# Optimization experiments

Hardware: AMD Instinct MI355X
Metric: run time of the kernel (lower is better)

## Reference

```python
import jax, jax.numpy as jnp
import numpy as np

K, N, MEM_D = 512, 4096, 64


def setup_inputs() -> dict:
    key = jax.random.key(0)
    k1, k2, k3, k4 = jax.random.split(key, 4)
    # event counts per location/time (torch code uses raw observations; rand in [0,1) keeps log-lik finite)
    obs = jax.random.uniform(k1, (K, N), jnp.float32)
    extobs = jax.random.normal(k2, (K, N), jnp.float32)
    beta = jnp.asarray(2.0, jnp.float32)  # torch.Tensor([2]) scalar rate parameter
    alpha = jax.random.uniform(k3, (K, K), jnp.float32, 0.0, 0.01)
    gamma = jax.random.uniform(k4, (K, MEM_D), jnp.float32, 0.0, 0.01)
    return {"obs": obs, "extobs": extobs, "beta": beta, "alpha": alpha, "gamma": gamma}


def reference(obs, extobs, beta, alpha, gamma):
    Kk, Nn = obs.shape
    d = gamma.shape[1]
    # mu is derived from obs exactly as in __init__ (not a trainable parameter)
    mu = obs.mean(axis=1) / 10.0 + 0.01  # [K]

    t = jnp.arange(Nn)
    diff = t[:, None] - t[None, :]  # [N, N], diff[t, j] = t - j
    # strict lower-triangular exponential decay kernel: D[t, j] = beta * exp(-(t-j)*beta) for j < t
    # clamp diff before exp so masked entries never produce inf (keeps vjp NaN-free)
    safe = jnp.maximum(diff, 1).astype(jnp.float32)
    Dmat = jnp.where(diff > 0, beta * jnp.exp(-safe * beta), 0.0)  # [N, N]

    # lam1[k, t] = sum_{k'} alpha[k, k'] * sum_{j < t} obs[k', j] * beta * exp(-(t-j)*beta)
    lam1 = alpha @ (obs @ Dmat.T)  # [K, N]

    # lam2[k, t] = sum_i extobs[k, t-d+i] * gamma[k, i]  (only when t >= d, else 0)
    # depthwise 1D cross-correlation with left zero-padding of d, then mask t < d
    x = extobs[None]            # [1, K, N]
    w = gamma[:, None, :]       # [K, 1, d]
    lam2 = jax.lax.conv_general_dilated(
        x, w, window_strides=(1,), padding=[(d, 0)],
        dimension_numbers=("NCH", "OIH", "NCH"), feature_group_count=Kk,
    )[0, :, :Nn]                # [K, N]
    lam2 = jnp.where(t[None, :] >= d, lam2, 0.0)

    lams = jax.nn.softplus(mu[:, None] + lam1 + lam2)  # [K, N]
    loglik = (obs * jnp.log(lams) - lams).sum()
    return (loglik, lams)
```

## Files before the change

kernel.cpp:

```cpp
#include <hip/hip_runtime.h>
#include <math.h>

#define KDIM 512
#define NDIM 4096
#define MEMD 64
#define WTAPS 16
#define SEG 1024
#define NSEG (NDIM / SEG)
#define NPART (KDIM * NSEG)

#define GBM 64
#define GBN 64
#define GBK 64

typedef short bf16x8 __attribute__((ext_vector_type(8)));
typedef float f32x4 __attribute__((ext_vector_type(4)));

#define GLOAD_LDS16(g, l) __builtin_amdgcn_global_load_lds( \
    (const __attribute__((address_space(1))) unsigned int*)(g), \
    (__attribute__((address_space(3))) unsigned int*)(l), 16, 0, 0)

__device__ __forceinline__ void bsplit(float a, ushort& hi, ushort& lo) {
    uint u = __float_as_uint(a);
    uint h = (u + 0x7FFFu + ((u >> 16) & 1u)) >> 16;
    hi = (ushort)h;
    float hf = __uint_as_float(h << 16);
    float r = a - hf;
    uint u2 = __float_as_uint(r);
    lo = (ushort)((u2 + 0x7FFFu + ((u2 >> 16) & 1u)) >> 16);
}

__device__ __forceinline__ float block_reduce_256(float v, float* sbuf) {
    #pragma unroll
    for (int off = 32; off > 0; off >>= 1) v += __shfl_down(v, off, 64);
    int lane = threadIdx.x & 63, wid = threadIdx.x >> 6;
    if (lane == 0) sbuf[wid] = v;
    __syncthreads();
    float tot = sbuf[0] + sbuf[1] + sbuf[2] + sbuf[3];
    __syncthreads();
    return tot;
}

__device__ __forceinline__ double block_reduce_256d(double v, double* dbuf) {
    #pragma unroll
    for (int off = 32; off > 0; off >>= 1) v += __shfl_down(v, off, 64);
    int lane = threadIdx.x & 63, wid = threadIdx.x >> 6;
    if (lane == 0) dbuf[wid] = v;
    __syncthreads();
    double tot = dbuf[0] + dbuf[1] + dbuf[2] + dbuf[3];
    __syncthreads();
    return tot;
}

__global__ __launch_bounds__(256) void conv_kernel(
    const float* __restrict__ B, const float* __restrict__ A,
    ushort* __restrict__ Bthi, ushort* __restrict__ Btlo,
    ushort* __restrict__ Ahi, ushort* __restrict__ Alo,
    float* __restrict__ mu) {
    __shared__ float s[64][65];
    int b = blockIdx.x, tid = threadIdx.x;
    if (b < 512) {
        int n0 = (b & 63) * 64, k0 = (b >> 6) * 64;
        #pragma unroll
        for (int i = 0; i < 4; ++i) {
            int idx = i * 256 + tid;
            int row = idx >> 4, c4 = idx & 15;
            float4 v = *(const float4*)&B[(size_t)(k0 + row) * NDIM + n0 + c4 * 4];
            s[row][c4 * 4 + 0] = v.x; s[row][c4 * 4 + 1] = v.y;
            s[row][c4 * 4 + 2] = v.z; s[row][c4 * 4 + 3] = v.w;
        }
        __syncthreads();
        #pragma unroll
        for (int i = 0; i < 2; ++i) {
            int idx = i * 256 + tid;
            int n = idx >> 3, k8 = idx & 7;
            ushort hs[8], ls[8];
            #pragma unroll
            for (int j = 0; j < 8; ++j) bsplit(s[k8 * 8 + j][n], hs[j], ls[j]);
            size_t o = (size_t)(n0 + n) * KDIM + k0 + k8 * 8;
            *(uint4*)&Bthi[o] = *(const uint4*)hs;
            *(uint4*)&Btlo[o] = *(const uint4*)ls;
        }
    } else if (b < 640) {
        int ab = b - 512;
        int g = ab * 256 + tid;
        const float4* src = (const float4*)A;
        #pragma unroll
        for (int i = 0; i < 2; ++i) {
            float4 v = src[g * 2 + i];
            ushort4 h, l;
            bsplit(v.x, h.x, l.x); bsplit(v.y, h.y, l.y);
            bsplit(v.z, h.z, l.z); bsplit(v.w, h.w, l.w);
            *(ushort4*)&Ahi[(size_t)g * 8 + i * 4] = h;
            *(ushort4*)&Alo[(size_t)g * 8 + i * 4] = l;
        }
    } else {
        int k = b - 640;
        const float* row = B + (size_t)k * NDIM;
        float ss = 0.f;
        for (int j = tid; j < NDIM; j += 256) ss += row[j];
        float tot = block_reduce_256(ss, &s[0][0]);
        if (tid == 0) mu[k] = tot / (float)NDIM / 10.0f + 0.01f;
    }
}

__global__ __launch_bounds__(256) void mfma_gemm(
    const ushort* __restrict__ Ahi, const ushort* __restrict__ Alo,
    const ushort* __restrict__ Bthi, const ushort* __restrict__ Btlo,
    float* __restrict__ C) {
    __shared__ __align__(16) ushort Asm[2][2][GBM * GBK];
    __shared__ __align__(16) ushort Bsm[2][2][GBN * GBK];
    int tid = threadIdx.x;
    int m0 = blockIdx.y * GBM, n0 = blockIdx.x * GBN;
    int l = tid & 63, w = tid >> 6;
    int wm = w >> 1, wn = w & 1;
    int lr = l & 15, lk = l >> 4;

    f32x4 acc[2][2];
    #pragma unroll
    for (int i = 0; i < 2; ++i)
        #pragma unroll
        for (int j = 0; j < 2; ++j) acc[i][j] = (f32x4){0.f, 0.f, 0.f, 0.f};

#define STAGE(bb, c0)                                                              \
    _Pragma("unroll")                                                              \
    for (int i_ = 0; i_ < 4; ++i_) {                                               \
        int c_ = tid + i_ * 256;                                                   \
        int plane_ = c_ >> 9, q_ = c_ & 511;                                       \
        int row_ = q_ >> 3, kc_ = (q_ & 7) ^ (row_ & 7);                           \
        const ushort* sa_ = (plane_ ? Alo : Ahi) + (size_t)(m0 + row_) * KDIM + (c0) + kc_ * 8; \
        GLOAD_LDS16(sa_, (char*)&Asm[bb][0][0] + c_ * 16);                         \
        const ushort* sb_ = (plane_ ? Btlo : Bthi) + (size_t)(n0 + row_) * KDIM + (c0) + kc_ * 8; \
        GLOAD_LDS16(sb_, (char*)&Bsm[bb][0][0] + c_ * 16);                         \
    }

    STAGE(0, 0);
    __syncthreads();

    for (int t = 0; t < 8; ++t) {
        int cur = t & 1;
        if (t < 7) { STAGE(cur ^ 1, (t + 1) * GBK); }

        bf16x8 ah[2][2], al[2][2], bh[2][2], bl[2][2];
        #pragma unroll
        for (int mf = 0; mf < 2; ++mf)
            #pragma unroll
            for (int s = 0; s < 2; ++s) {
                int ra = wm * 32 + mf * 16 + lr;
                int offa = ra * 128 + (((s * 64) + lk * 16) ^ ((ra & 7) << 4));
                ah[mf][s] = *(const bf16x8*)((const char*)&Asm[cur][0][0] + offa);
                al[mf][s] = *(const bf16x8*)((const char*)&Asm[cur][1][0] + offa);
                int rb = wn * 32 + mf * 16 + lr;
                int offb = rb * 128 + (((s * 64) + lk * 16) ^ ((rb & 7) << 4));
                bh[mf][s] = *(const bf16x8*)((const char*)&Bsm[cur][0][0] + offb);
                bl[mf][s] = *(const bf16x8*)((const char*)&Bsm[cur][1][0] + offb);
            }
        #pragma unroll
        for (int s = 0; s < 2; ++s)
            #pragma unroll
            for (int mf = 0; mf < 2; ++mf)
                #pragma unroll
                for (int nf = 0; nf < 2; ++nf) {
                    acc[mf][nf] = __builtin_amdgcn_mfma_f32_16x16x32_bf16(ah[mf][s], bh[nf][s], acc[mf][nf], 0, 0, 0);
                    acc[mf][nf] = __builtin_amdgcn_mfma_f32_16x16x32_bf16(ah[mf][s], bl[nf][s], acc[mf][nf], 0, 0, 0);
                    acc[mf][nf] = __builtin_amdgcn_mfma_f32_16x16x32_bf16(al[mf][s], bh[nf][s], acc[mf][nf], 0, 0, 0);
                }
        __syncthreads();
    }
#undef STAGE

    #pragma unroll
    for (int mf = 0; mf < 2; ++mf)
        #pragma unroll
        for (int nf = 0; nf < 2; ++nf)
            #pragma unroll
            for (int j = 0; j < 4; ++j) {
                int rm = m0 + wm * 32 + mf * 16 + lk * 4 + j;
                int cn = n0 + wn * 32 + nf * 16 + lr;
                C[(size_t)rm * NDIM + cn] = acc[mf][nf][j];
            }
}

__global__ __launch_bounds__(256) void final_kernel(
    const float* __restrict__ T, const float* __restrict__ obs,
    const float* __restrict__ extobs, const float* __restrict__ gamma,
    const float* __restrict__ beta_p, const float* __restrict__ mu,
    float* __restrict__ lams_out, double* __restrict__ partials) {
    __shared__ float Ts[SEG + 16];
    __shared__ float Es[SEG + 64];
    __shared__ float Os[SEG];
    __shared__ float Gs[MEMD];
    __shared__ float Wt[WTAPS];
    __shared__ double dbuf[4];

    int b = blockIdx.x, tid = threadIdx.x;
    int k = b >> 2, s = b & 3;
    float beta = *beta_p;
    float muk = mu[k];

    const float4* gT = (const float4*)(T + (size_t)k * NDIM);
    const float4* gE = (const float4*)(extobs + (size_t)k * NDIM);
    const float4* gO = (const float4*)(obs + (size_t)k * NDIM);
    float4 z = make_float4(0.f, 0.f, 0.f, 0.f);

    {
        for (int i = tid; i < 260; i += 256) {
            int gi = s * 256 - 4 + i;
            ((float4*)Ts)[i] = (gi >= 0) ? gT[gi] : z;
        }
        for (int i = tid; i < 272; i += 256) {
            int gi = s * 256 - 16 + i;
            ((float4*)Es)[i] = (gi >= 0) ? gE[gi] : z;
        }
        ((float4*)Os)[tid] = gO[s * 256 + tid];
        if (tid < MEMD) Gs[tid] = gamma[(size_t)k * MEMD + tid];
        if (tid >= 64 && tid < 64 + WTAPS) {
            int m = tid - 63;
            Wt[m - 1] = beta * expf(-beta * (float)m);
        }
    }
    __syncthreads();

    int t_loc = tid * 4;
    int t = s * SEG + t_loc;
    float win[20];
    float l1[4] = {0.f, 0.f, 0.f, 0.f};
    float l2[4] = {0.f, 0.f, 0.f, 0.f};

    #pragma unroll
    for (int c = 0; c < 5; ++c) *(float4*)&win[c * 4] = *(const float4*)&Ts[t_loc + c * 4];
    #pragma unroll
    for (int m = 1; m <= WTAPS; ++m) {
        float wm = Wt[m - 1];
        #pragma unroll
        for (int j = 0; j < 4; ++j) l1[j] = fmaf(wm, win[16 + j - m], l1[j]);
    }

    #pragma unroll
    for (int c4 = 0; c4 < 4; ++c4) {
        #pragma unroll
        for (int c = 0; c < 5; ++c)
            *(float4*)&win[c * 4] = *(const float4*)&Es[t_loc + c4 * 16 + c * 4];
        #pragma unroll
        for (int i = 0; i < 16; ++i) {
            float g = Gs[c4 * 16 + i];
            #pragma unroll
            for (int j = 0; j < 4; ++j) l2[j] = fmaf(g, win[i + j], l2[j]);
        }
    }
    if (t < MEMD) { l2[0] = 0.f; l2[1] = 0.f; l2[2] = 0.f; l2[3] = 0.f; }

    float4 o = ((const float4*)Os)[tid];
    float oo[4] = {o.x, o.y, o.z, o.w};
    double part = 0.0;
    f32x4 sv;
    #pragma unroll
    for (int j = 0; j < 4; ++j) {
        float x = muk + l1[j] + l2[j];
        float sp = fmaxf(x, 0.f) + log1pf(expf(-fabsf(x)));
        sv[j] = sp;
        part += (double)(oo[j] * logf(sp) - sp);
    }
    *(f32x4*)&lams_out[(size_t)k * NDIM + t] = sv;

    double dtot = block_reduce_256d(part, dbuf);
    if (tid == 0) partials[b] = dtot;
}

__global__ __launch_bounds__(256) void reduce_kernel(const double* __restrict__ partials,
                                                     float* __restrict__ out) {
    __shared__ double dbuf[4];
    double v = 0.0;
    for (int j = threadIdx.x; j < NPART; j += 256) v += partials[j];
    double tot = block_reduce_256d(v, dbuf);
    if (threadIdx.x == 0) out[0] = (float)tot;
}

extern "C" void kernel_launch(void* const* d_in, const int* in_sizes, int n_in,
                              void* d_out, int out_size, void* d_ws, size_t ws_size,
                              hipStream_t stream) {
    const float* obs    = (const float*)d_in[0];
    const float* extobs = (const float*)d_in[1];
    const float* beta   = (const float*)d_in[2];
    const float* alpha  = (const float*)d_in[3];
    const float* gamma  = (const float*)d_in[4];
    float* out = (float*)d_out;

    char* ws = (char*)d_ws;
    float*  T        = (float*)(ws);
    ushort* Bthi     = (ushort*)(ws + (8u << 20));
    ushort* Btlo     = (ushort*)(ws + (12u << 20));
    ushort* Ahi      = (ushort*)(ws + (16u << 20));
    ushort* Alo      = (ushort*)(ws + (16u << 20) + (512u << 10));
    double* partials = (double*)(ws + (17u << 20));
    float* mu        = (float*)(ws + (17u << 20) + (32u << 10));

    conv_kernel<<<512 + 128 + 512, 256, 0, stream>>>(obs, alpha, Bthi, Btlo,
                                                     Ahi, Alo, mu);
    mfma_gemm<<<dim3(NDIM / GBN, KDIM / GBM), 256, 0, stream>>>(Ahi, Alo, Bthi, Btlo, T);
    final_kernel<<<NPART, 256, 0, stream>>>(T, obs, extobs, gamma, beta, mu,
                                            out + 1, partials);
    reduce_kernel<<<1, 256, 0, stream>>>(partials, out);
}
```

Baseline: 115.0 us.

## Process all row segments per block with register-staged double-buffered prefetch

The final kernel now runs one block per row k that loops over the four 1024-element segments, instead of one block per segment. While the current segment is computed from shared memory, the next segment's T, extobs and obs data is prefetched into registers and then written into the alternate shared buffer. This is meant to hide global load latency and cut the number of partials the reduce kernel reads. The grid shrinks from 2048 to 512 blocks, so there is less block-level parallelism to hide latency, and register and LDS use per block go up.

```diff
diff --git a/kernel.cpp b/kernel.cpp
--- a/kernel.cpp
+++ b/kernel.cpp
@@ -7,7 +7,6 @@
 #define WTAPS 16
 #define SEG 1024
 #define NSEG (NDIM / SEG)
-#define NPART (KDIM * NSEG)
 
 #define GBM 64
 #define GBN 64
@@ -186,15 +185,14 @@
     const float* __restrict__ extobs, const float* __restrict__ gamma,
     const float* __restrict__ beta_p, const float* __restrict__ mu,
     float* __restrict__ lams_out, double* __restrict__ partials) {
-    __shared__ float Ts[SEG + 16];
-    __shared__ float Es[SEG + 64];
-    __shared__ float Os[SEG];
+    __shared__ float Ts[2][SEG + 16];
+    __shared__ float Es[2][SEG + 64];
+    __shared__ float Os[2][SEG];
     __shared__ float Gs[MEMD];
     __shared__ float Wt[WTAPS];
     __shared__ double dbuf[4];
 
-    int b = blockIdx.x, tid = threadIdx.x;
-    int k = b >> 2, s = b & 3;
+    int k = blockIdx.x, tid = threadIdx.x;
     float beta = *beta_p;
     float muk = mu[k];
 
@@ -203,75 +201,100 @@
     const float4* gO = (const float4*)(obs + (size_t)k * NDIM);
     float4 z = make_float4(0.f, 0.f, 0.f, 0.f);
 
-    {
-        for (int i = tid; i < 260; i += 256) {
-            int gi = s * 256 - 4 + i;
-            ((float4*)Ts)[i] = (gi >= 0) ? gT[gi] : z;
-        }
-        for (int i = tid; i < 272; i += 256) {
-            int gi = s * 256 - 16 + i;
-            ((float4*)Es)[i] = (gi >= 0) ? gE[gi] : z;
-        }
-        ((float4*)Os)[tid] = gO[s * 256 + tid];
-        if (tid < MEMD) Gs[tid] = gamma[(size_t)k * MEMD + tid];
-        if (tid >= 64 && tid < 64 + WTAPS) {
-            int m = tid - 63;
-            Wt[m - 1] = beta * expf(-beta * (float)m);
-        }
-    }
-    __syncthreads();
-
+    for (int i = tid; i < 260; i += 256) {
+        int gi = i - 4;
+        ((float4*)Ts[0])[i] = (gi >= 0) ? gT[gi] : z;
+    }
+    for (int i = tid; i < 272; i += 256) {
+        int gi = i - 16;
+        ((float4*)Es[0])[i] = (gi >= 0) ? gE[gi] : z;
+    }
+    ((float4*)Os[0])[tid] = gO[tid];
+    if (tid < MEMD) Gs[tid] = gamma[(size_t)k * MEMD + tid];
+    if (tid >= 64 && tid < 64 + WTAPS) {
+        int m = tid - 63;
+        Wt[m - 1] = beta * expf(-beta * (float)m);
+    }
+    __syncthreads();
+
+    double part = 0.0;
     int t_loc = tid * 4;
-    int t = s * SEG + t_loc;
-    float win[20];
-    float l1[4] = {0.f, 0.f, 0.f, 0.f};
-    float l2[4] = {0.f, 0.f, 0.f, 0.f};
-
-    #pragma unroll
-    for (int c = 0; c < 5; ++c) *(float4*)&win[c * 4] = *(const float4*)&Ts[t_loc + c * 4];
-    #pragma unroll
-    for (int m = 1; m <= WTAPS; ++m) {
-        float wm = Wt[m - 1];
-        #pragma unroll
-        for (int j = 0; j < 4; ++j) l1[j] = fmaf(wm, win[16 + j - m], l1[j]);
-    }
-
-    #pragma unroll
-    for (int c4 = 0; c4 < 4; ++c4) {
+
+    #pragma unroll
+    for (int s = 0; s < NSEG; ++s) {
+        int cur = s & 1;
+
+        float4 rT0, rT1, rE0, rE1, rO;
+        if (s < NSEG - 1) {
+            int base = (s + 1) * 256;
+            rT0 = gT[base - 4 + tid];
+            if (tid < 4)  rT1 = gT[base + 252 + tid];
+            rE0 = gE[base - 16 + tid];
+            if (tid < 16) rE1 = gE[base + 240 + tid];
+            rO  = gO[base + tid];
+        }
+
+        int t = s * SEG + t_loc;
+        float win[20];
+        float l1[4] = {0.f, 0.f, 0.f, 0.f};
+        float l2[4] = {0.f, 0.f, 0.f, 0.f};
+
         #pragma unroll
         for (int c = 0; c < 5; ++c)
-            *(float4*)&win[c * 4] = *(const float4*)&Es[t_loc + c4 * 16 + c * 4];
-        #pragma unroll
-        for (int i = 0; i < 16; ++i) {
-            float g = Gs[c4 * 16 + i];
-            #pragma unroll
-            for (int j = 0; j < 4; ++j) l2[j] = fmaf(g, win[i + j], l2[j]);
-        }
-    }
-    if (t < MEMD) { l2[0] = 0.f; l2[1] = 0.f; l2[2] = 0.f; l2[3] = 0.f; }
-
-    float4 o = ((const float4*)Os)[tid];
-    float oo[4] = {o.x, o.y, o.z, o.w};
-    double part = 0.0;
-    f32x4 sv;
-    #pragma unroll
-    for (int j = 0; j < 4; ++j) {
-        float x = muk + l1[j] + l2[j];
-        float sp = fmaxf(x, 0.f) + log1pf(expf(-fabsf(x)));
-        sv[j] = sp;
-        part += (double)(oo[j] * logf(sp) - sp);
-    }
-    *(f32x4*)&lams_out[(size_t)k * NDIM + t] = sv;
+            *(float4*)&win[c * 4] = *(const float4*)&Ts[cur][t_loc + c * 4];
+        #pragma unroll
+        for (int m = 1; m <= WTAPS; ++m) {
+            float wm = Wt[m - 1];
+            #pragma unroll
+            for (int j = 0; j < 4; ++j) l1[j] = fmaf(wm, win[16 + j - m], l1[j]);
+        }
+
+        #pragma unroll
+        for (int c4 = 0; c4 < 4; ++c4) {
+            #pragma unroll
+            for (int c = 0; c < 5; ++c)
+                *(float4*)&win[c * 4] = *(const float4*)&Es[cur][t_loc + c4 * 16 + c * 4];
+            #pragma unroll
+            for (int i = 0; i < 16; ++i) {
+                float g = Gs[c4 * 16 + i];
+                #pragma unroll
+                for (int j = 0; j < 4; ++j) l2[j] = fmaf(g, win[i + j], l2[j]);
+            }
+        }
+        if (t < MEMD) { l2[0] = 0.f; l2[1] = 0.f; l2[2] = 0.f; l2[3] = 0.f; }
+
+        float4 o = ((const float4*)Os[cur])[tid];
+        float oo[4] = {o.x, o.y, o.z, o.w};
+        f32x4 sv;
+        #pragma unroll
+        for (int j = 0; j < 4; ++j) {
+            float x = muk + l1[j] + l2[j];
+            float sp = fmaxf(x, 0.f) + log1pf(expf(-fabsf(x)));
+            sv[j] = sp;
+            part += (double)(oo[j] * logf(sp) - sp);
+        }
+        *(f32x4*)&lams_out[(size_t)k * NDIM + t] = sv;
+
+        if (s < NSEG - 1) {
+            int nxt = cur ^ 1;
+            ((float4*)Ts[nxt])[tid] = rT0;
+            if (tid < 4)  ((float4*)Ts[nxt])[256 + tid] = rT1;
+            ((float4*)Es[nxt])[tid] = rE0;
+            if (tid < 16) ((float4*)Es[nxt])[256 + tid] = rE1;
+            ((float4*)Os[nxt])[tid] = rO;
+            __syncthreads();
+        }
+    }
 
     double dtot = block_reduce_256d(part, dbuf);
-    if (tid == 0) partials[b] = dtot;
+    if (tid == 0) partials[k] = dtot;
 }
 
 __global__ __launch_bounds__(256) void reduce_kernel(const double* __restrict__ partials,
                                                      float* __restrict__ out) {
     __shared__ double dbuf[4];
     double v = 0.0;
-    for (int j = threadIdx.x; j < NPART; j += 256) v += partials[j];
+    for (int j = threadIdx.x; j < KDIM; j += 256) v += partials[j];
     double tot = block_reduce_256d(v, dbuf);
     if (threadIdx.x == 0) out[0] = (float)tot;
 }
@@ -298,7 +321,7 @@
     conv_kernel<<<512 + 128 + 512, 256, 0, stream>>>(obs, alpha, Bthi, Btlo,
                                                      Ahi, Alo, mu);
     mfma_gemm<<<dim3(NDIM / GBN, KDIM / GBM), 256, 0, stream>>>(Ahi, Alo, Bthi, Btlo, T);
-    final_kernel<<<NPART, 256, 0, stream>>>(T, obs, extobs, gamma, beta, mu,
-                                            out + 1, partials);
+    final_kernel<<<KDIM, 256, 0, stream>>>(T, obs, extobs, gamma, beta, mu,
+                                           out + 1, partials);
     reduce_kernel<<<1, 256, 0, stream>>>(partials, out);
 }
```

New measurement: 109.6 us. 1.05x faster.
